# Kernel optimization log

Measured on AMD Instinct MI355X. Metric: run time of the kernel, lower is better.

## Reference

```python
import jax, jax.numpy as jnp
import numpy as np

STRIDE = 16   # compression_stride
CBLK = 32     # compression_block
SBLK = 64     # selection_block
NSEL = 16     # selected_block_count
WIN = 512     # sliding_window


def _masked_softmax(s, mask):
    neg = jnp.finfo(s.dtype).min
    sm = jnp.where(mask, s, neg)
    m = jnp.max(sm, axis=-1, keepdims=True)
    e = jnp.where(mask, jnp.exp(sm - m), 0.0)
    return e / jnp.maximum(jnp.sum(e, axis=-1, keepdims=True), 1e-20)


def _nsa_forward(q, k, v, Wk_cmp, Wv_cmp, Wg, bg, bs, S):
    total, HQ, D = q.shape
    HK, Dv = k.shape[1], v.shape[2]
    G = HQ // HK  # GQA group size
    scale = 1.0 / jnp.sqrt(jnp.float32(D))
    # [bs, HK, G, S, D] grouped query layout, [bs, HK, S, D] kv layout
    q5 = q.reshape(bs, S, HQ, D).transpose(0, 2, 1, 3).reshape(bs, HK, G, S, D)
    k4 = k.reshape(bs, S, HK, D).transpose(0, 2, 1, 3)
    v4 = v.reshape(bs, S, HK, Dv).transpose(0, 2, 1, 3)

    # ---- compressed KV (learned linear over each sliding window) ----
    C = (S - CBLK) // STRIDE + 1
    starts = jnp.arange(C) * STRIDE
    widx = starts[:, None] + jnp.arange(CBLK)           # [C, CBLK]
    ck = jnp.einsum('bhcwd,wde->bhce', k4[:, :, widx, :], Wk_cmp)  # [bs,HK,C,D]
    cv = jnp.einsum('bhcwd,wde->bhce', v4[:, :, widx, :], Wv_cmp)

    # ---- compressed attention (causal on fully-past blocks) ----
    t = jnp.arange(S)
    cmask = (starts[None, :] + CBLK) <= (t[:, None] + 1)  # [S, C]
    sc = jnp.einsum('bhgsd,bhcd->bhgsc', q5, ck) * scale
    pc = _masked_softmax(sc, cmask[None, None, None])     # [bs,HK,G,S,C]
    cmp_o = jnp.einsum('bhgsc,bhce->bhgse', pc, cv)

    # ---- block-selection scores: sum over GQA group, AvgPool1d(5,4,0,ceil) ----
    score = pc.sum(2)                                     # [bs,HK,S,C]
    KP = SBLK // STRIDE + 1
    PS = SBLK // STRIDE
    Nblk = S // SBLK
    pidx = jnp.arange(Nblk)[:, None] * PS + jnp.arange(KP)  # [Nblk,KP]
    pv = pidx < C
    g = jnp.where(pv, score[..., jnp.clip(pidx, 0, C - 1)], 0.0)
    pooled = g.sum(-1) / pv.sum(-1).astype(jnp.float32)   # [bs,HK,S,Nblk]
    idx = jax.lax.top_k(pooled, NSEL)[1]                  # [bs,HK,S,NSEL]
    sel_blk = (idx[..., None] == jnp.arange(Nblk)).any(-2)  # [bs,HK,S,Nblk]
    tok_sel = jnp.take(sel_blk, t // SBLK, axis=-1)        # [bs,HK,S,S]

    # ---- selected-block attention and sliding-window attention ----
    causal = t[:, None] >= t[None, :]
    raw = jnp.einsum('bhgsd,bhtd->bhgst', q5, k4) * scale  # [bs,HK,G,S,S]
    sel_o = jnp.einsum('bhgst,bhte->bhgse',
                       _masked_softmax(raw, (tok_sel & causal)[:, :, None]), v4)
    wmask = causal & ((t[:, None] - t[None, :]) < WIN)
    win_o = jnp.einsum('bhgst,bhte->bhgse',
                       _masked_softmax(raw, wmask[None, None, None]), v4)

    # ---- learned gate over the three paths ----
    gate = jax.nn.sigmoid(jnp.einsum('bhgsd,de->bhgse', q5, Wg) + bg)
    o = gate[..., 0:1] * sel_o + gate[..., 1:2] * win_o + gate[..., 2:3] * cmp_o
    return o.reshape(bs, HQ, S, Dv).transpose(0, 2, 1, 3).reshape(total, HQ, Dv)


def setup_inputs() -> dict:
    key = jax.random.key(0)
    ks = jax.random.split(key, 6)
    S, HQ, HK, D = 2048, 16, 4, 128
    total = 1 * S
    q = jax.random.normal(ks[0], (total, HQ, D), jnp.float32)
    k = jax.random.normal(ks[1], (total, HK, D), jnp.float32)
    v = jax.random.normal(ks[2], (total, HK, D), jnp.float32)
    Wk_cmp = jax.random.normal(ks[3], (CBLK, D, D), jnp.float32) * 0.02
    Wv_cmp = jax.random.normal(ks[4], (CBLK, D, D), jnp.float32) * 0.02
    Wg = jax.random.normal(ks[5], (D, 3), jnp.float32) * 0.02
    bg = jnp.zeros((3,), jnp.float32)
    cu_seqlens = jnp.array([0, S], jnp.int32)
    return {"q": q, "k": k, "v": v, "Wk_cmp": Wk_cmp, "Wv_cmp": Wv_cmp,
            "Wg": Wg, "bg": bg, "cu_seqlens": cu_seqlens, "max_seqlen": S}


def reference(q, k, v, Wk_cmp, Wv_cmp, Wg, bg, cu_seqlens, max_seqlen):
    bs = cu_seqlens.shape[0] - 1
    S = q.shape[0] // bs
    return _nsa_forward(q, k, v, Wk_cmp, Wv_cmp, Wg, bg, bs, S)
```

## Files before the change

### kernel.cpp

```cpp
#include <hip/hip_runtime.h>
#include <math.h>

#define HQn 16
#define HKn 4
#define Gn 4
#define Dn 128
#define STRIDEn 16
#define CBLKn 32
#define SBLKn 64
#define NSELn 16
#define WINn 512
#define Sn 2048
#define Cn 127
#define NBLKn 32

typedef float f32x4 __attribute__((ext_vector_type(4)));
typedef __bf16 bf16x8 __attribute__((ext_vector_type(8)));
typedef unsigned short ushort8 __attribute__((ext_vector_type(8)));
typedef unsigned int uint2v __attribute__((ext_vector_type(2)));

__device__ inline f32x4 mfma16(bf16x8 a, bf16x8 b, f32x4 c) {
  return __builtin_amdgcn_mfma_f32_16x16x32_bf16(a, b, c, 0, 0, 0);
}
__device__ inline unsigned short f2bfu(float x) {
  return __builtin_bit_cast(unsigned short, (__bf16)x);
}
__device__ inline unsigned pk2(float a, float b) {
  return (unsigned)f2bfu(a) | ((unsigned)f2bfu(b) << 16);
}
__device__ inline void gll16(const void* g, void* l) {
  __builtin_amdgcn_global_load_lds(
      (const __attribute__((address_space(1))) unsigned*)g,
      (__attribute__((address_space(3))) unsigned*)l, 16, 0, 0);
}

__global__ __launch_bounds__(256)
void nsa_cvtq(const float* __restrict__ q, const float* __restrict__ k,
              unsigned short* __restrict__ qbf, unsigned short* __restrict__ kbf) {
  const float scale = 0.08838834764831845f;
  const int gid = blockIdx.x * 256 + threadIdx.x;
  if (gid < 524288) {
    const size_t i = (size_t)gid * 8;
    const float4* s = (const float4*)(q + i);
    float4 a = s[0], b = s[1];
    ushort8 u;
    u[0]=f2bfu(a.x*scale); u[1]=f2bfu(a.y*scale); u[2]=f2bfu(a.z*scale); u[3]=f2bfu(a.w*scale);
    u[4]=f2bfu(b.x*scale); u[5]=f2bfu(b.y*scale); u[6]=f2bfu(b.z*scale); u[7]=f2bfu(b.w*scale);
    *(ushort8*)(qbf + i) = u;
  } else {
    const int g2 = gid - 524288;
    const size_t o = (size_t)g2 * 8;
    const int hk = (int)(o >> 18);
    const int r  = (int)(o & 262143);
    const int t = r >> 7, d = r & 127;
    const float4* s = (const float4*)(k + ((size_t)t * 4 + hk) * 128 + d);
    float4 a = s[0], b = s[1];
    ushort8 u;
    u[0]=f2bfu(a.x); u[1]=f2bfu(a.y); u[2]=f2bfu(a.z); u[3]=f2bfu(a.w);
    u[4]=f2bfu(b.x); u[5]=f2bfu(b.y); u[6]=f2bfu(b.z); u[7]=f2bfu(b.w);
    *(ushort8*)(kbf + o) = u;
  }
}

__global__ __launch_bounds__(256)
void nsa_cvtv(const float* __restrict__ v, unsigned short* __restrict__ vtb) {
  __shared__ __align__(16) unsigned short tile[64][136];
  const int tid = threadIdx.x;
  const int tb = blockIdx.x * 64, hk = blockIdx.y;
  {
    const int tl = tid >> 2, dc = (tid & 3) * 32;
    const float4* src = (const float4*)(v + ((size_t)(tb + tl) * 4 + hk) * 128 + dc);
#pragma unroll
    for (int ii = 0; ii < 4; ++ii) {
      float4 a = src[ii * 2], b = src[ii * 2 + 1];
      ushort8 u;
      u[0]=f2bfu(a.x); u[1]=f2bfu(a.y); u[2]=f2bfu(a.z); u[3]=f2bfu(a.w);
      u[4]=f2bfu(b.x); u[5]=f2bfu(b.y); u[6]=f2bfu(b.z); u[7]=f2bfu(b.w);
      *(ushort8*)&tile[tl][dc + ii * 8] = u;
    }
  }
  __syncthreads();
  {
    const int d = tid >> 1, th = tid & 1;
    ushort8 u[4];
#pragma unroll
    for (int ii = 0; ii < 4; ++ii)
#pragma unroll
      for (int t = 0; t < 8; ++t)
        u[ii][t] = tile[th * 32 + ii * 8 + t][d];
    ushort8* dst = (ushort8*)(vtb + (size_t)hk * 262144 + (size_t)d * 2048 + tb + th * 32);
#pragma unroll
    for (int ii = 0; ii < 4; ++ii) dst[ii] = u[ii];
  }
}

__global__ __launch_bounds__(512)
void nsa_compress(const float* __restrict__ k, const float* __restrict__ v,
                  const float* __restrict__ Wk, const float* __restrict__ Wv,
                  float* __restrict__ part) {
  const int wf = blockIdx.z;
  const int which = wf >> 2, fs = wf & 3;
  const int hk = blockIdx.y;
  const int c = blockIdx.x * 16 + (threadIdx.x >> 5);
  const int e0 = (threadIdx.x & 31) * 4;
  if (c >= Cn) return;
  const float* src = which ? v : k;
  const float* W = which ? Wv : Wk;
  float a0 = 0.f, a1 = 0.f, a2 = 0.f, a3 = 0.f;
  const int w0 = fs * 8;
  for (int wi = 0; wi < 8; ++wi) {
    const int row = c * STRIDEn + w0 + wi;
    const float4* kr = (const float4*)(src + ((size_t)row * HKn + hk) * Dn);
    const float* Wr = W + (size_t)(w0 + wi) * Dn * Dn;
#pragma unroll 4
    for (int d4 = 0; d4 < 32; ++d4) {
      float4 kk = kr[d4];
      float4 w0v = *(const float4*)(Wr + (size_t)(d4 * 4 + 0) * Dn + e0);
      float4 w1v = *(const float4*)(Wr + (size_t)(d4 * 4 + 1) * Dn + e0);
      float4 w2v = *(const float4*)(Wr + (size_t)(d4 * 4 + 2) * Dn + e0);
      float4 w3v = *(const float4*)(Wr + (size_t)(d4 * 4 + 3) * Dn + e0);
      a0 += kk.x * w0v.x + kk.y * w1v.x + kk.z * w2v.x + kk.w * w3v.x;
      a1 += kk.x * w0v.y + kk.y * w1v.y + kk.z * w2v.y + kk.w * w3v.y;
      a2 += kk.x * w0v.z + kk.y * w1v.z + kk.z * w2v.z + kk.w * w3v.z;
      a3 += kk.x * w0v.w + kk.y * w1v.w + kk.z * w2v.w + kk.w * w3v.w;
    }
  }
  float* d = part + (size_t)(which * 4 + fs) * (HKn * Cn * Dn)
                  + ((size_t)hk * Cn + c) * Dn + e0;
  d[0] = a0; d[1] = a1; d[2] = a2; d[3] = a3;
}

__global__ void nsa_reduce(const float* __restrict__ part,
                           float* __restrict__ ck, float* __restrict__ cv) {
  const int i = blockIdx.x * 256 + threadIdx.x;
  const int N = HKn * Cn * Dn;
  if (i < N) {
    ck[i] = ((part[i] + part[(size_t)N + i]) + (part[2 * (size_t)N + i] + part[3 * (size_t)N + i]));
    cv[i] = ((part[4 * (size_t)N + i] + part[5 * (size_t)N + i]) + (part[6 * (size_t)N + i] + part[7 * (size_t)N + i]));
  }
}

__global__ __launch_bounds__(256)
void nsa_cmp_sel(const float* __restrict__ q, const float* __restrict__ ck,
                 const float* __restrict__ cv, const float* __restrict__ Wg,
                 const float* __restrict__ bg, float* __restrict__ gates,
                 unsigned long long* __restrict__ selm, float* __restrict__ out) {
  __shared__ float pcs2[4][128][4];
  __shared__ float score_l[4][128];
  __shared__ float gate2_l[4][Gn];
  const int wid = threadIdx.x >> 6, lane = threadIdx.x & 63;
  const int s = blockIdx.x * 4 + wid;
  const int hk = blockIdx.y;
  const float scale = 0.08838834764831845f;
  const int cmax = (s >= CBLKn - 1) ? ((s - (CBLKn - 1)) >> 4) + 1 : 0;

  const float4* qg = (const float4*)(q + ((size_t)s * HQn + hk * Gn) * Dn);
  const int c1l = (lane + 64 < Cn) ? lane + 64 : Cn - 1;
  const float4* k0p = (const float4*)(ck + ((size_t)hk * Cn + lane) * Dn);
  const float4* k1p = (const float4*)(ck + ((size_t)hk * Cn + c1l) * Dn);
  float a00=0,a01=0,a10=0,a11=0,a20=0,a21=0,a30=0,a31=0;
#pragma unroll 8
  for (int d4 = 0; d4 < 32; ++d4) {
    const float4 k0 = k0p[d4], k1 = k1p[d4];
    const float4 q0 = qg[0*32 + d4], q1 = qg[1*32 + d4];
    const float4 q2 = qg[2*32 + d4], q3 = qg[3*32 + d4];
    a00 += k0.x*q0.x + k0.y*q0.y + k0.z*q0.z + k0.w*q0.w;
    a01 += k1.x*q0.x + k1.y*q0.y + k1.z*q0.z + k1.w*q0.w;
    a10 += k0.x*q1.x + k0.y*q1.y + k0.z*q1.z + k0.w*q1.w;
    a11 += k1.x*q1.x + k1.y*q1.y + k1.z*q1.z + k1.w*q1.w;
    a20 += k0.x*q2.x + k0.y*q2.y + k0.z*q2.z + k0.w*q2.w;
    a21 += k1.x*q2.x + k1.y*q2.y + k1.z*q2.z + k1.w*q2.w;
    a30 += k0.x*q3.x + k0.y*q3.y + k0.z*q3.z + k0.w*q3.w;
    a31 += k1.x*q3.x + k1.y*q3.y + k1.z*q3.z + k1.w*q3.w;
  }
  float x0[4] = {a00*scale, a10*scale, a20*scale, a30*scale};
  float x1[4] = {a01*scale, a11*scale, a21*scale, a31*scale};

  float p0[4], p1[4];
#pragma unroll
  for (int g = 0; g < 4; ++g) {
    float m = -1e30f;
    if (lane < cmax) m = x0[g];
    if (lane + 64 < cmax) m = fmaxf(m, x1[g]);
    for (int off = 32; off; off >>= 1) m = fmaxf(m, __shfl_xor(m, off));
    float e0v = (lane < cmax) ? __expf(x0[g] - m) : 0.f;
    float e1v = (lane + 64 < cmax) ? __expf(x1[g] - m) : 0.f;
    float sum = e0v + e1v;
    for (int off = 32; off; off >>= 1) sum += __shfl_xor(sum, off);
    float inv = 1.f / fmaxf(sum, 1e-20f);
    p0[g] = e0v * inv; p1[g] = e1v * inv;
  }
  {
    float4 v0 = {p0[0], p0[1], p0[2], p0[3]};
    float4 v1 = {p1[0], p1[1], p1[2], p1[3]};
    *(float4*)&pcs2[wid][lane][0] = v0;
    *(float4*)&pcs2[wid][lane + 64][0] = v1;
    score_l[wid][lane] = v0.x + v0.y + v0.z + v0.w;
    score_l[wid][lane + 64] = v1.x + v1.y + v1.z + v1.w;
  }
  float pooled; int myj;
  if (lane < NBLKn) {
    myj = lane; float sum = 0.f; int cnt = 0;
    for (int kp = 0; kp <= 4; ++kp) {
      int idx = lane * 4 + kp;
      if (idx < Cn) { sum += score_l[wid][idx]; cnt++; }
    }
    pooled = sum / (float)cnt;
  } else { myj = 63; pooled = -INFINITY; }
  unsigned long long msk = 0ull;
  for (int r = 0; r < NSELn; ++r) {
    float bv = pooled; int bi = myj;
    for (int off = 32; off; off >>= 1) {
      float ov = __shfl_xor(bv, off); int oi = __shfl_xor(bi, off);
      if (ov > bv || (ov == bv && oi < bi)) { bv = ov; bi = oi; }
    }
    msk |= (1ull << bi);
    if (myj == bi) pooled = -INFINITY;
  }
  if (lane == 0) selm[(size_t)s * HKn + hk] = msk;

  if (lane < 48) {
    const int gj = lane >> 2, ch = lane & 3;
    const int g = gj / 3, jj = gj % 3;
    const float* qrow = q + ((size_t)s * HQn + hk * Gn + g) * Dn;
    float a = 0.f;
#pragma unroll 8
    for (int d = ch * 32; d < ch * 32 + 32; ++d) a += qrow[d] * Wg[d * 3 + jj];
    a += __shfl_xor(a, 1); a += __shfl_xor(a, 2);
    if (ch == 0) {
      const float gv = 1.f / (1.f + __expf(-(a + bg[jj])));
      gates[((size_t)s * HQn + hk * Gn + g) * 3 + jj] = gv;
      if (jj == 2) gate2_l[wid][g] = gv;
    }
  }

  {
    float b0[4] = {0,0,0,0}, b1[4] = {0,0,0,0};
    float c0a[4] = {0,0,0,0}, c1a[4] = {0,0,0,0};
    int cc = 0;
    for (; cc + 2 <= cmax; cc += 2) {
      float4 pp = *(const float4*)&pcs2[wid][cc][0];
      float4 qq = *(const float4*)&pcs2[wid][cc + 1][0];
      float va1 = cv[((size_t)hk * Cn + cc) * Dn + lane];
      float va2 = cv[((size_t)hk * Cn + cc) * Dn + lane + 64];
      float vb1 = cv[((size_t)hk * Cn + cc + 1) * Dn + lane];
      float vb2 = cv[((size_t)hk * Cn + cc + 1) * Dn + lane + 64];
      b0[0] += pp.x*va1; b0[1] += pp.y*va1; b0[2] += pp.z*va1; b0[3] += pp.w*va1;
      b1[0] += pp.x*va2; b1[1] += pp.y*va2; b1[2] += pp.z*va2; b1[3] += pp.w*va2;
      c0a[0] += qq.x*vb1; c0a[1] += qq.y*vb1; c0a[2] += qq.z*vb1; c0a[3] += qq.w*vb1;
      c1a[0] += qq.x*vb2; c1a[1] += qq.y*vb2; c1a[2] += qq.z*vb2; c1a[3] += qq.w*vb2;
    }
    if (cc < cmax) {
      float4 pp = *(const float4*)&pcs2[wid][cc][0];
      float va1 = cv[((size_t)hk * Cn + cc) * Dn + lane];
      float va2 = cv[((size_t)hk * Cn + cc) * Dn + lane + 64];
      b0[0] += pp.x*va1; b0[1] += pp.y*va1; b0[2] += pp.z*va1; b0[3] += pp.w*va1;
      b1[0] += pp.x*va2; b1[1] += pp.y*va2; b1[2] += pp.z*va2; b1[3] += pp.w*va2;
    }
#pragma unroll
    for (int g = 0; g < 4; ++g) {
      float g2 = gate2_l[wid][g];
      out[((size_t)s * HQn + hk * Gn + g) * Dn + lane] = g2 * (b0[g] + c0a[g]);
      out[((size_t)s * HQn + hk * Gn + g) * Dn + lane + 64] = g2 * (b1[g] + c1a[g]);
    }
  }
}

__device__ inline void stage_tile(const char* kh, const char* vh, int tb,
                                  char* kb, char* vb, int tid) {
#pragma unroll
  for (int i = 0; i < 4; ++i) {
    const int L = i * 4096 + tid * 16;
    const int row = L >> 8, colb = L & 255;
    gll16(kh + ((size_t)(tb + row) << 8) + (colb ^ ((row & 7) << 4)), kb + L);
  }
#pragma unroll
  for (int i = 0; i < 4; ++i) {
    const int L = i * 4096 + tid * 16;
    const int e = L >> 7, colb = L & 127;
    gll16(vh + ((size_t)e << 12) + ((size_t)tb << 1) + (colb ^ ((e & 7) << 4)), vb + L);
  }
}

__global__ __launch_bounds__(256, 2)
void nsa_attn(const unsigned short* __restrict__ qbf,
              const unsigned short* __restrict__ kbf,
              const unsigned short* __restrict__ vtb,
              const float* __restrict__ gates,
              const unsigned long long* __restrict__ selm,
              float* __restrict__ out) {
  __shared__ __align__(16) char sK[2][16384];
  __shared__ __align__(16) char sV[2][16384];
  __shared__ __align__(16) char sP[4][2048];

  const int tid = threadIdx.x, lane = tid & 63, w = tid >> 6;
  const int cl = lane & 15, h4 = lane >> 4;
  const int swzb = (blockIdx.x & 7) * 64 + (blockIdx.x >> 3);
  const int s0 = (swzb & 127) * 16;
  const int hk = swzb >> 7;
  const int srow = s0 + cl;
  const int head = hk * Gn + w;
  const int swz = (cl & 7) << 4;

  const unsigned long long mymask = selm[(size_t)srow * HKn + hk];
  unsigned long long un = mymask;
  un |= __shfl_xor(un, 1); un |= __shfl_xor(un, 2);
  un |= __shfl_xor(un, 4); un |= __shfl_xor(un, 8);

  const int jmax = (s0 + 15) >> 6;
  const int jw0 = (s0 >= WINn - 1) ? (s0 - (WINn - 1)) >> 6 : 0;
  const unsigned long long allm = (2ull << jmax) - 1;

  const char* kh = (const char*)kbf + ((size_t)hk << 19);
  const char* vh = (const char*)vtb + ((size_t)hk << 19);

  bf16x8 qb[4];
#pragma unroll
  for (int ks = 0; ks < 4; ++ks)
    qb[ks] = *(const bf16x8*)((const char*)qbf +
        ((size_t)srow * HQn + head) * 256 + ks * 64 + h4 * 16);
  const float g0 = gates[((size_t)srow * HQn + head) * 3 + 0];
  const float g1 = gates[((size_t)srow * HQn + head) * 3 + 1];
  float* orow = out + ((size_t)srow * HQn + head) * Dn;

  for (int ph = 0; ph < 2; ++ph) {
    unsigned long long nm = ph ? (allm & ~((1ull << jw0) - 1)) : (un & allm);
    float m = -1e30f, den = 0.f;
    f32x4 O[8];
#pragma unroll
    for (int ef = 0; ef < 8; ++ef) { f32x4 z = {0.f,0.f,0.f,0.f}; O[ef] = z; }

    if (nm) {
      int j = (int)__builtin_ctzll(nm); nm &= nm - 1;
      stage_tile(kh, vh, j * 64, (char*)sK[0], (char*)sV[0], tid);
      __syncthreads();
      int cur = 0;
      while (true) {
        int jn = -1;
        if (nm) {
          jn = (int)__builtin_ctzll(nm); nm &= nm - 1;
          stage_tile(kh, vh, jn * 64, (char*)sK[cur ^ 1], (char*)sV[cur ^ 1], tid);
        }
        const int tb = j * 64;
        float xr[16];
#pragma unroll
        for (int mt = 0; mt < 4; ++mt) {
          f32x4 acc = {0.f, 0.f, 0.f, 0.f};
#pragma unroll
          for (int ks = 0; ks < 4; ++ks) {
            const int row = mt * 16 + cl;
            const bf16x8 ka = *(const bf16x8*)(sK[cur] + row * 256 +
                ((unsigned)(ks * 64 + h4 * 16) ^ swz));
            acc = mfma16(ka, qb[ks], acc);
          }
          xr[4*mt+0] = acc[0]; xr[4*mt+1] = acc[1];
          xr[4*mt+2] = acc[2]; xr[4*mt+3] = acc[3];
        }
        const bool selb = (mymask >> j) & 1ull;
        unsigned vm = 0u;
#pragma unroll
        for (int i = 0; i < 16; ++i) {
          const int token = tb + (i >> 2) * 16 + h4 * 4 + (i & 3);
          const bool cz = token <= srow;
          const bool ok = ph ? (cz && (srow - token) < WINn) : (cz && selb);
          if (ok) vm |= (1u << i);
        }
        float bm = -1e30f;
#pragma unroll
        for (int i = 0; i < 16; ++i) if ((vm >> i) & 1u) bm = fmaxf(bm, xr[i]);
        bm = fmaxf(bm, __shfl_xor(bm, 16));
        bm = fmaxf(bm, __shfl_xor(bm, 32));
        if (bm > m + 8.f) {
          const float sc = __expf(m - bm);
#pragma unroll
          for (int ef = 0; ef < 8; ++ef) O[ef] *= sc;
          den *= sc; m = bm;
        }
#pragma unroll
        for (int i = 0; i < 16; ++i) xr[i] = __expf(xr[i] - m);
#pragma unroll
        for (int i = 0; i < 16; ++i) den += ((vm >> i) & 1u) ? xr[i] : 0.f;
#pragma unroll
        for (int mt = 0; mt < 4; ++mt) {
          const float p0 = ((vm >> (4*mt+0)) & 1u) ? xr[4*mt+0] : 0.f;
          const float p1 = ((vm >> (4*mt+1)) & 1u) ? xr[4*mt+1] : 0.f;
          const float p2 = ((vm >> (4*mt+2)) & 1u) ? xr[4*mt+2] : 0.f;
          const float p3 = ((vm >> (4*mt+3)) & 1u) ? xr[4*mt+3] : 0.f;
          uint2v u; u[0] = pk2(p0, p1); u[1] = pk2(p2, p3);
          *(uint2v*)(sP[w] + cl * 128 + ((unsigned)(mt * 32 + h4 * 8) ^ swz)) = u;
        }
#pragma unroll
        for (int kt = 0; kt < 2; ++kt) {
          const bf16x8 f = *(const bf16x8*)(sP[w] + cl * 128 +
              ((unsigned)(kt * 64 + h4 * 16) ^ swz));
#pragma unroll
          for (int ef = 0; ef < 8; ++ef) {
            const int vrow = ef * 16 + cl;
            const bf16x8 vf = *(const bf16x8*)(sV[cur] + vrow * 128 +
                ((unsigned)(kt * 64 + h4 * 16) ^ swz));
            O[ef] = mfma16(vf, f, O[ef]);
          }
        }
        __syncthreads();
        if (jn < 0) break;
        j = jn; cur ^= 1;
      }
    }
    den += __shfl_xor(den, 16); den += __shfl_xor(den, 32);
    const float c = (ph ? g1 : g0) / fmaxf(den, 1e-20f);
#pragma unroll
    for (int ef = 0; ef < 8; ++ef) {
      float4* p = (float4*)(orow + ef * 16 + h4 * 4);
      float4 o = *p;
      o.x += c * O[ef][0];
      o.y += c * O[ef][1];
      o.z += c * O[ef][2];
      o.w += c * O[ef][3];
      *p = o;
    }
  }
}

extern "C" void kernel_launch(void* const* d_in, const int* in_sizes, int n_in,
                              void* d_out, int out_size, void* d_ws, size_t ws_size,
                              hipStream_t stream) {
  const float* q  = (const float*)d_in[0];
  const float* k  = (const float*)d_in[1];
  const float* v  = (const float*)d_in[2];
  const float* Wk = (const float*)d_in[3];
  const float* Wv = (const float*)d_in[4];
  const float* Wg = (const float*)d_in[5];
  const float* bg = (const float*)d_in[6];
  float* out = (float*)d_out;

  const int N = HKn * Cn * Dn;
  float* part  = (float*)d_ws;
  float* ck    = part + (size_t)8 * N;
  float* cv    = ck + N;
  float* gates = cv + N;
  unsigned long long* selm = (unsigned long long*)(gates + (size_t)Sn * HQn * 3);
  unsigned short* qbf = (unsigned short*)(selm + (size_t)Sn * HKn);
  unsigned short* kbf = qbf + (size_t)Sn * HQn * Dn;
  unsigned short* vtb = kbf + (size_t)Sn * HKn * Dn;

  nsa_cvtq<<<2560, 256, 0, stream>>>(q, k, qbf, kbf);
  nsa_cvtv<<<dim3(32, HKn), 256, 0, stream>>>(v, vtb);
  nsa_compress<<<dim3(8, HKn, 8), 512, 0, stream>>>(k, v, Wk, Wv, part);
  nsa_reduce<<<dim3((N + 255) / 256), 256, 0, stream>>>(part, ck, cv);
  nsa_cmp_sel<<<dim3(Sn / 4, HKn), 256, 0, stream>>>(q, ck, cv, Wg, bg, gates, selm, out);
  nsa_attn<<<512, 256, 0, stream>>>(qbf, kbf, vtb, gates, selm, out);
}
```

Measured before the change: 394.4 us.

## Transpose compressed keys, stage q in LDS, and use rank-based top-k selection

The reduce kernel now also writes a transposed copy of the compressed keys ([hk][d][c]), so the compressed-score loop in nsa_cmp_sel reads coalesced scalars per lane instead of strided float4 rows. Each wave stages its four query rows in shared memory and reuses them for the gate projection. The second half of the compressed blocks is only computed when cmax exceeds 64. The 16-round shuffle argmax top-k is replaced by a per-lane rank count over shared pooled scores and a ballot. The cost is extra LDS use, an extra transposed write in the reduce kernel, and more workspace.

```diff
diff --git a/kernel.cpp b/kernel.cpp
--- a/kernel.cpp
+++ b/kernel.cpp
@@ -131,50 +131,83 @@
 }
 
 __global__ void nsa_reduce(const float* __restrict__ part,
-                           float* __restrict__ ck, float* __restrict__ cv) {
+                           float* __restrict__ ck, float* __restrict__ cv,
+                           float* __restrict__ ckt) {
   const int i = blockIdx.x * 256 + threadIdx.x;
   const int N = HKn * Cn * Dn;
   if (i < N) {
-    ck[i] = ((part[i] + part[(size_t)N + i]) + (part[2 * (size_t)N + i] + part[3 * (size_t)N + i]));
+    const float kv = ((part[i] + part[(size_t)N + i]) + (part[2 * (size_t)N + i] + part[3 * (size_t)N + i]));
+    ck[i] = kv;
     cv[i] = ((part[4 * (size_t)N + i] + part[5 * (size_t)N + i]) + (part[6 * (size_t)N + i] + part[7 * (size_t)N + i]));
+    const int hk = i / (Cn * Dn);
+    const int r  = i - hk * (Cn * Dn);
+    const int c  = r >> 7, d = r & 127;
+    ckt[((size_t)hk * Dn + d) * 128 + c] = kv;
   }
 }
 
 __global__ __launch_bounds__(256)
-void nsa_cmp_sel(const float* __restrict__ q, const float* __restrict__ ck,
+void nsa_cmp_sel(const float* __restrict__ q, const float* __restrict__ ckt,
                  const float* __restrict__ cv, const float* __restrict__ Wg,
                  const float* __restrict__ bg, float* __restrict__ gates,
                  unsigned long long* __restrict__ selm, float* __restrict__ out) {
   __shared__ float pcs2[4][128][4];
   __shared__ float score_l[4][128];
   __shared__ float gate2_l[4][Gn];
+  __shared__ float pool_l[4][32];
+  __shared__ __align__(16) float qs_l[4][Gn][Dn];
   const int wid = threadIdx.x >> 6, lane = threadIdx.x & 63;
   const int s = blockIdx.x * 4 + wid;
   const int hk = blockIdx.y;
   const float scale = 0.08838834764831845f;
   const int cmax = (s >= CBLKn - 1) ? ((s - (CBLKn - 1)) >> 4) + 1 : 0;
 
-  const float4* qg = (const float4*)(q + ((size_t)s * HQn + hk * Gn) * Dn);
+  {
+    const float4* qg = (const float4*)(q + ((size_t)s * HQn + hk * Gn) * Dn);
+    float4* dst = (float4*)&qs_l[wid][0][0];
+    dst[lane] = qg[lane];
+    dst[lane + 64] = qg[lane + 64];
+  }
+
+  const float* ckt_h = ckt + (size_t)hk * Dn * 128;
   const int c1l = (lane + 64 < Cn) ? lane + 64 : Cn - 1;
-  const float4* k0p = (const float4*)(ck + ((size_t)hk * Cn + lane) * Dn);
-  const float4* k1p = (const float4*)(ck + ((size_t)hk * Cn + c1l) * Dn);
-  float a00=0,a01=0,a10=0,a11=0,a20=0,a21=0,a30=0,a31=0;
+  float a00=0,a10=0,a20=0,a30=0;
 #pragma unroll 8
   for (int d4 = 0; d4 < 32; ++d4) {
-    const float4 k0 = k0p[d4], k1 = k1p[d4];
-    const float4 q0 = qg[0*32 + d4], q1 = qg[1*32 + d4];
-    const float4 q2 = qg[2*32 + d4], q3 = qg[3*32 + d4];
-    a00 += k0.x*q0.x + k0.y*q0.y + k0.z*q0.z + k0.w*q0.w;
-    a01 += k1.x*q0.x + k1.y*q0.y + k1.z*q0.z + k1.w*q0.w;
-    a10 += k0.x*q1.x + k0.y*q1.y + k0.z*q1.z + k0.w*q1.w;
-    a11 += k1.x*q1.x + k1.y*q1.y + k1.z*q1.z + k1.w*q1.w;
-    a20 += k0.x*q2.x + k0.y*q2.y + k0.z*q2.z + k0.w*q2.w;
-    a21 += k1.x*q2.x + k1.y*q2.y + k1.z*q2.z + k1.w*q2.w;
-    a30 += k0.x*q3.x + k0.y*q3.y + k0.z*q3.z + k0.w*q3.w;
-    a31 += k1.x*q3.x + k1.y*q3.y + k1.z*q3.z + k1.w*q3.w;
+    const float kx = ckt_h[(d4 * 4 + 0) * 128 + lane];
+    const float ky = ckt_h[(d4 * 4 + 1) * 128 + lane];
+    const float kz = ckt_h[(d4 * 4 + 2) * 128 + lane];
+    const float kw = ckt_h[(d4 * 4 + 3) * 128 + lane];
+    const float4 q0 = *(const float4*)&qs_l[wid][0][d4 * 4];
+    const float4 q1 = *(const float4*)&qs_l[wid][1][d4 * 4];
+    const float4 q2 = *(const float4*)&qs_l[wid][2][d4 * 4];
+    const float4 q3 = *(const float4*)&qs_l[wid][3][d4 * 4];
+    a00 += kx*q0.x + ky*q0.y + kz*q0.z + kw*q0.w;
+    a10 += kx*q1.x + ky*q1.y + kz*q1.z + kw*q1.w;
+    a20 += kx*q2.x + ky*q2.y + kz*q2.z + kw*q2.w;
+    a30 += kx*q3.x + ky*q3.y + kz*q3.z + kw*q3.w;
   }
   float x0[4] = {a00*scale, a10*scale, a20*scale, a30*scale};
-  float x1[4] = {a01*scale, a11*scale, a21*scale, a31*scale};
+  float x1[4] = {-1e30f, -1e30f, -1e30f, -1e30f};
+  if (cmax > 64) {
+    float a01=0,a11=0,a21=0,a31=0;
+#pragma unroll 8
+    for (int d4 = 0; d4 < 32; ++d4) {
+      const float kx = ckt_h[(d4 * 4 + 0) * 128 + c1l];
+      const float ky = ckt_h[(d4 * 4 + 1) * 128 + c1l];
+      const float kz = ckt_h[(d4 * 4 + 2) * 128 + c1l];
+      const float kw = ckt_h[(d4 * 4 + 3) * 128 + c1l];
+      const float4 q0 = *(const float4*)&qs_l[wid][0][d4 * 4];
+      const float4 q1 = *(const float4*)&qs_l[wid][1][d4 * 4];
+      const float4 q2 = *(const float4*)&qs_l[wid][2][d4 * 4];
+      const float4 q3 = *(const float4*)&qs_l[wid][3][d4 * 4];
+      a01 += kx*q0.x + ky*q0.y + kz*q0.z + kw*q0.w;
+      a11 += kx*q1.x + ky*q1.y + kz*q1.z + kw*q1.w;
+      a21 += kx*q2.x + ky*q2.y + kz*q2.z + kw*q2.w;
+      a31 += kx*q3.x + ky*q3.y + kz*q3.z + kw*q3.w;
+    }
+    x1[0]=a01*scale; x1[1]=a11*scale; x1[2]=a21*scale; x1[3]=a31*scale;
+  }
 
   float p0[4], p1[4];
 #pragma unroll
@@ -198,34 +231,34 @@
     score_l[wid][lane] = v0.x + v0.y + v0.z + v0.w;
     score_l[wid][lane + 64] = v1.x + v1.y + v1.z + v1.w;
   }
-  float pooled; int myj;
+
+  float pooled = -INFINITY;
   if (lane < NBLKn) {
-    myj = lane; float sum = 0.f; int cnt = 0;
+    float sum = 0.f; int cnt = 0;
     for (int kp = 0; kp <= 4; ++kp) {
       int idx = lane * 4 + kp;
       if (idx < Cn) { sum += score_l[wid][idx]; cnt++; }
     }
     pooled = sum / (float)cnt;
-  } else { myj = 63; pooled = -INFINITY; }
-  unsigned long long msk = 0ull;
-  for (int r = 0; r < NSELn; ++r) {
-    float bv = pooled; int bi = myj;
-    for (int off = 32; off; off >>= 1) {
-      float ov = __shfl_xor(bv, off); int oi = __shfl_xor(bi, off);
-      if (ov > bv || (ov == bv && oi < bi)) { bv = ov; bi = oi; }
-    }
-    msk |= (1ull << bi);
-    if (myj == bi) pooled = -INFINITY;
-  }
+    pool_l[wid][lane] = pooled;
+  }
+  int rank = 0;
+  if (lane < NBLKn) {
+#pragma unroll
+    for (int i = 0; i < NBLKn; ++i) {
+      const float vi = pool_l[wid][i];
+      rank += (vi > pooled || (vi == pooled && i < lane)) ? 1 : 0;
+    }
+  }
+  const unsigned long long msk = __ballot(lane < NBLKn && rank < NSELn);
   if (lane == 0) selm[(size_t)s * HKn + hk] = msk;
 
   if (lane < 48) {
     const int gj = lane >> 2, ch = lane & 3;
     const int g = gj / 3, jj = gj % 3;
-    const float* qrow = q + ((size_t)s * HQn + hk * Gn + g) * Dn;
     float a = 0.f;
 #pragma unroll 8
-    for (int d = ch * 32; d < ch * 32 + 32; ++d) a += qrow[d] * Wg[d * 3 + jj];
+    for (int d = ch * 32; d < ch * 32 + 32; ++d) a += qs_l[wid][g][d] * Wg[d * 3 + jj];
     a += __shfl_xor(a, 1); a += __shfl_xor(a, 2);
     if (ch == 0) {
       const float gv = 1.f / (1.f + __expf(-(a + bg[jj])));
@@ -442,11 +475,12 @@
   unsigned short* qbf = (unsigned short*)(selm + (size_t)Sn * HKn);
   unsigned short* kbf = qbf + (size_t)Sn * HQn * Dn;
   unsigned short* vtb = kbf + (size_t)Sn * HKn * Dn;
+  float* ckt = (float*)(vtb + (size_t)Sn * HKn * Dn);
 
   nsa_cvtq<<<2560, 256, 0, stream>>>(q, k, qbf, kbf);
   nsa_cvtv<<<dim3(32, HKn), 256, 0, stream>>>(v, vtb);
   nsa_compress<<<dim3(8, HKn, 8), 512, 0, stream>>>(k, v, Wk, Wv, part);
-  nsa_reduce<<<dim3((N + 255) / 256), 256, 0, stream>>>(part, ck, cv);
-  nsa_cmp_sel<<<dim3(Sn / 4, HKn), 256, 0, stream>>>(q, ck, cv, Wg, bg, gates, selm, out);
+  nsa_reduce<<<dim3((N + 255) / 256), 256, 0, stream>>>(part, ck, cv, ckt);
+  nsa_cmp_sel<<<dim3(Sn / 4, HKn), 256, 0, stream>>>(q, ckt, cv, Wg, bg, gates, selm, out);
   nsa_attn<<<512, 256, 0, stream>>>(qbf, kbf, vtb, gates, selm, out);
 }
```

Result: faster. 321.2 us (-18.6%).
